# Performance work log

Measured on AMD Instinct MI355X. Metric: run time of the kernel, lower is better.

## Reference

```python
import jax, jax.numpy as jnp
import numpy as np

N = 100000   # nodes
R = 8        # relations
E = 150000   # edges per relation
D_IN = 128
D_OUT = 128
B = 2        # num_bases


def setup_inputs() -> dict:
    key = jax.random.key(0)
    ks = jax.random.split(key, 7)
    return {
        "x": jax.random.normal(ks[0], (N, D_IN), dtype=jnp.float32),
        "src": jax.random.randint(ks[1], (R, E), 0, N, dtype=jnp.int32),
        "dst": jax.random.randint(ks[2], (R, E), 0, N, dtype=jnp.int32),
        "basis_coeff": jax.random.normal(ks[3], (R, B), dtype=jnp.float32),
        "bases": jax.random.normal(ks[4], (B, D_IN, D_OUT), dtype=jnp.float32) * 0.05,
        "loop_weight": jax.random.normal(ks[5], (D_IN, D_OUT), dtype=jnp.float32) * 0.05,
        "h_bias": jax.random.normal(ks[6], (D_OUT,), dtype=jnp.float32) * 0.01,
    }


def reference(x, src, dst, basis_coeff, bases, loop_weight, h_bias):
    n = x.shape[0]
    # basis-decomposed per-relation weights: [R, D_IN, D_OUT]
    weight = jnp.einsum('rb,bio->rio', basis_coeff, bases)
    # gather src features per relation: [R, E, D_IN]
    msgs = x[src]
    # scatter-add onto dst nodes per relation (SpMM aggregate): [R, N, D_IN]
    agg = jax.vmap(lambda m, d: jax.ops.segment_sum(m, d, num_segments=n))(msgs, dst)
    # right normalization: divide by in-degree (clamped to 1), as in DGL GraphConv norm='right'
    ones = jnp.ones(src.shape[1], dtype=x.dtype)
    deg = jax.vmap(lambda d: jax.ops.segment_sum(ones, d, num_segments=n))(dst)
    agg = agg / jnp.clip(deg, 1.0)[..., None]
    # per-relation weight then sum across relations (HeteroGraphConv 'sum' agg)
    h = jnp.einsum('rni,rio->no', agg, weight)
    # self-loop + bias + activation (dropout = 0.0, eval)
    h = h + x @ loop_weight + h_bias
    return jax.nn.relu(h)
```

## Files before the change

### kernel.cpp

```cpp
#include <hip/hip_runtime.h>
#include <hip/hip_fp16.h>


#define DFEAT 128
#define NREL 8
#define ALDA 264
#define ECAP 512

typedef __attribute__((ext_vector_type(8))) short bf16x8;
typedef __attribute__((ext_vector_type(4))) float f32x4;
typedef __attribute__((ext_vector_type(2))) float f32x2;

__device__ __forceinline__ ushort f2bf(float f) {
    unsigned u = __float_as_uint(f);
    u += 0x7FFF + ((u >> 16) & 1);
    return (ushort)(u >> 16);
}
__device__ __forceinline__ float bflo(unsigned u) { return __uint_as_float(u << 16); }
__device__ __forceinline__ float bfhi(unsigned u) { return __uint_as_float(u & 0xFFFF0000u); }
__device__ __forceinline__ unsigned pack2bf(float lo, float hi) {
    return (unsigned)f2bf(lo) | ((unsigned)f2bf(hi) << 16);
}

__global__ void fused_pre(const int* __restrict__ dst, int* __restrict__ deg,
                          ushort* __restrict__ rank,
                          const float* __restrict__ x, ushort* __restrict__ xb,
                          const float* __restrict__ bases, const float* __restrict__ loopw,
                          ushort* __restrict__ w2T,
                          int RE, int E, int N, int n4) {
    const int stride = gridDim.x * blockDim.x;
    const int t0 = blockIdx.x * blockDim.x + threadIdx.x;
    for (int i = t0; i < RE; i += stride) {
        int r = i / E;
        int d = dst[i];
        rank[i] = (ushort)atomicAdd(&deg[r * N + d], 1);
    }
    for (int i = t0; i < n4; i += stride) {
        float4 v = ((const float4*)x)[i];
        ushort4 o;
        o.x = f2bf(v.x); o.y = f2bf(v.y); o.z = f2bf(v.z); o.w = f2bf(v.w);
        ((ushort4*)xb)[i] = o;
    }
    for (int i = t0; i < 128 * 384; i += stride) {
        int j = i / 384, k = i % 384;
        float v = (k < 256) ? bases[(k >> 7) * DFEAT * DFEAT + (k & 127) * DFEAT + j]
                            : loopw[(k - 256) * DFEAT + j];
        w2T[i] = f2bf(v);
    }
}

__global__ void scan_block_sums(const int* __restrict__ deg,
                                int* __restrict__ bsums, int N) {
    __shared__ int sdata[256];
    int b = blockIdx.x, t = threadIdx.x;
    int idx = b * 256 + t;
    int sum = 0;
    if (idx < N) {
        #pragma unroll
        for (int r = 0; r < NREL; ++r) sum += deg[r * N + idx];
    }
    sdata[t] = sum; __syncthreads();
    for (int s = 128; s > 0; s >>= 1) {
        if (t < s) sdata[t] += sdata[t + s];
        __syncthreads();
    }
    if (t == 0) bsums[b] = sdata[0];
}

__global__ void scan_write(const int* __restrict__ bsums,
                           const int* __restrict__ deg,
                           int* __restrict__ rowStart, unsigned* __restrict__ packed,
                           int N) {
    __shared__ int sdata[256];
    int b = blockIdx.x, t = threadIdx.x;

    int part = 0;
    for (int k = t; k < b; k += 256) part += bsums[k];
    sdata[t] = part; __syncthreads();
    for (int s = 128; s > 0; s >>= 1) {
        if (t < s) sdata[t] += sdata[t + s];
        __syncthreads();
    }
    const int boff = sdata[0];
    __syncthreads();

    int idx = b * 256 + t;
    int dvs[NREL];
    int c = 0;
    if (idx < N) {
        #pragma unroll
        for (int r = 0; r < NREL; ++r) { dvs[r] = deg[r * N + idx]; c += dvs[r]; }
    }
    sdata[t] = c; __syncthreads();
    for (int off = 1; off < 256; off <<= 1) {
        int x = 0;
        if (t >= off) x = sdata[t - off];
        __syncthreads();
        if (t >= off) sdata[t] += x;
        __syncthreads();
    }
    int excl = sdata[t] - c;
    if (idx < N) {
        int rs = boff + excl;
        rowStart[idx] = rs;
        int pre = 0;
        #pragma unroll
        for (int r = 0; r < NREL; ++r) {
            int dv = dvs[r];
            packed[r * N + idx] = ((unsigned)(rs + pre) << 11) | (unsigned)dv;
            pre += dv;
        }
    }
}

__global__ void fill_kernel(const int* __restrict__ src, const int* __restrict__ dst,
                            const ushort* __restrict__ rank,
                            const unsigned* __restrict__ packed,
                            unsigned* __restrict__ recs, int RE, int E, int N) {
    int idx = blockIdx.x * blockDim.x + threadIdx.x;
    if (idx >= RE) return;
    int r = idx / E;
    int d = dst[idx];
    unsigned p = packed[r * N + d];
    int pos = (int)(p >> 11) + (int)rank[idx];
    recs[pos] = (unsigned)src[idx] | ((unsigned)r << 17);
}

__global__ __launch_bounds__(256, 7) void gather_gemm(
    const unsigned* __restrict__ recs, const int* __restrict__ rowStart,
    const int* __restrict__ deg, const float* __restrict__ coeff,
    const ushort* __restrict__ xb,
    const ushort* __restrict__ w2T, const float* __restrict__ bias,
    float* __restrict__ out, int N, int RE) {
    __shared__ __align__(16) ushort agg[32 * ALDA];
    __shared__ __align__(16) unsigned recsL[ECAP];
    __shared__ float2 ccL[32 * NREL];
    __shared__ int rsl[33];
    const int tid = threadIdx.x;
    const int wave = tid >> 6, lane = tid & 63;
    const int row0 = blockIdx.x * 32;

    if (tid < 33) {
        int d = row0 + tid;
        rsl[tid] = (d < N) ? rowStart[d] : RE;
    }
    {
        int i = tid & 31, r = tid >> 5;
        int d = row0 + i;
        float2 cc = {0.f, 0.f};
        if (d < N) {
            int dv = deg[r * N + d];
            float inv = (dv > 0) ? 1.0f / (float)dv : 0.f;
            cc.x = coeff[2 * r] * inv;
            cc.y = coeff[2 * r + 1] * inv;
        }
        ccL[i * NREL + r] = cc;
    }
    __syncthreads();
    const int e0 = rsl[0];
    const int cntE = rsl[32] - e0;
    const bool fits = (cntE <= ECAP);
    {
        const int lim = fits ? cntE : 0;
        for (int k = tid; k < lim; k += 256)
            recsL[k] = recs[e0 + k];
    }
    __syncthreads();

    {
        const int qw = tid >> 4;
        const int h  = tid & 15;

        auto gatherNode = [&](int i, auto getRec) {
            const int s   = rsl[i] - e0;
            const int len = rsl[i + 1] - rsl[i];
            f32x2 A0 = {0.f,0.f}, A1 = {0.f,0.f}, A2 = {0.f,0.f}, A3 = {0.f,0.f};
            f32x2 B0 = {0.f,0.f}, B1 = {0.f,0.f}, B2 = {0.f,0.f}, B3 = {0.f,0.f};
            if (len > 0) {
                const int last = s + len - 1;
                for (int k = 0; k < len; k += 8) {
                    unsigned rc[8];
                    #pragma unroll
                    for (int j = 0; j < 8; ++j) {
                        int li = s + k + j;
                        rc[j] = getRec(li <= last ? li : last);
                    }
                    uint4 u[8];
                    #pragma unroll
                    for (int j = 0; j < 8; ++j)
                        u[j] = *(const uint4*)(xb + (size_t)(rc[j] & 0x1FFFFu) * DFEAT + h * 8);
                    #pragma unroll
                    for (int j = 0; j < 8; ++j) {
                        bool v = (k + j) < len;
                        float2 cf = ccL[i * NREL + (rc[j] >> 17)];
                        float c0 = v ? cf.x : 0.f;
                        float c1 = v ? cf.y : 0.f;
                        f32x2 cc0 = {c0, c0}, cc1 = {c1, c1};
                        uint4 uu = u[j];
                        f32x2 f01 = {bflo(uu.x), bfhi(uu.x)};
                        f32x2 f23 = {bflo(uu.y), bfhi(uu.y)};
                        f32x2 f45 = {bflo(uu.z), bfhi(uu.z)};
                        f32x2 f67 = {bflo(uu.w), bfhi(uu.w)};
                        A0 += cc0 * f01; A1 += cc0 * f23; A2 += cc0 * f45; A3 += cc0 * f67;
                        B0 += cc1 * f01; B1 += cc1 * f23; B2 += cc1 * f45; B3 += cc1 * f67;
                    }
                }
            }
            uint4 w0, w1;
            w0.x = pack2bf(A0.x, A0.y); w0.y = pack2bf(A1.x, A1.y);
            w0.z = pack2bf(A2.x, A2.y); w0.w = pack2bf(A3.x, A3.y);
            w1.x = pack2bf(B0.x, B0.y); w1.y = pack2bf(B1.x, B1.y);
            w1.z = pack2bf(B2.x, B2.y); w1.w = pack2bf(B3.x, B3.y);
            *(uint4*)(agg + i * ALDA + h * 8)       = w0;
            *(uint4*)(agg + i * ALDA + 128 + h * 8) = w1;
        };

        if (fits) {
            #pragma unroll
            for (int p = 0; p < 2; ++p)
                gatherNode(qw + p * 16, [&](int li) { return recsL[li]; });
        } else {
            #pragma unroll
            for (int p = 0; p < 2; ++p)
                gatherNode(qw + p * 16, [&](int li) { return recs[e0 + li]; });
        }
    }
    __syncthreads();

    const int quad = lane >> 4, l16 = lane & 15;
    int arow[2];
    #pragma unroll
    for (int m = 0; m < 2; ++m) {
        int r = row0 + m * 16 + l16;
        arow[m] = (r < N) ? r : 0;
    }

    f32x4 zero = {0.f, 0.f, 0.f, 0.f};
    f32x4 acc[2][2] = {{zero, zero}, {zero, zero}};

    #pragma unroll
    for (int kt = 0; kt < 3; ++kt) {
        bf16x8 bq[4][2];
        #pragma unroll
        for (int t = 0; t < 4; ++t)
            #pragma unroll
            for (int g = 0; g < 2; ++g)
                bq[t][g] = *(const bf16x8*)(w2T + (size_t)(wave * 32 + g * 16 + l16) * 384
                                            + kt * 128 + t * 32 + quad * 8);
        #pragma unroll
        for (int m = 0; m < 2; ++m) {
            #pragma unroll
            for (int t = 0; t < 4; ++t) {
                bf16x8 a;
                if (kt < 2)
                    a = *(const bf16x8*)(agg + (m * 16 + l16) * ALDA + kt * 128 + t * 32 + quad * 8);
                else
                    a = *(const bf16x8*)(xb + (size_t)arow[m] * DFEAT + t * 32 + quad * 8);
                acc[m][0] = __builtin_amdgcn_mfma_f32_16x16x32_bf16(a, bq[t][0], acc[m][0], 0, 0, 0);
                acc[m][1] = __builtin_amdgcn_mfma_f32_16x16x32_bf16(a, bq[t][1], acc[m][1], 0, 0, 0);
            }
        }
    }

    #pragma unroll
    for (int g = 0; g < 2; ++g) {
        int c = wave * 32 + g * 16 + l16;
        float bv = bias[c];
        #pragma unroll
        for (int m = 0; m < 2; ++m) {
            #pragma unroll
            for (int reg = 0; reg < 4; ++reg) {
                int grow = row0 + m * 16 + quad * 4 + reg;
                if (grow < N)
                    out[(size_t)grow * DFEAT + c] = fmaxf(acc[m][g][reg] + bv, 0.f);
            }
        }
    }
}

extern "C" void kernel_launch(void* const* d_in, const int* in_sizes, int n_in,
                              void* d_out, int out_size, void* d_ws, size_t ws_size,
                              hipStream_t stream) {
    const float* x     = (const float*)d_in[0];
    const int*   src   = (const int*)  d_in[1];
    const int*   dst   = (const int*)  d_in[2];
    const float* coeff = (const float*)d_in[3];
    const float* bases = (const float*)d_in[4];
    const float* loopw = (const float*)d_in[5];
    const float* bias  = (const float*)d_in[6];
    float* out = (float*)d_out;

    const int N  = in_sizes[0] / DFEAT;
    const int RE = in_sizes[1];
    const int B  = in_sizes[4] / (DFEAT * DFEAT);
    const int R  = in_sizes[3] / B;
    const int E  = RE / R;
    const int NB = (N + 255) / 256;
    const int n4 = N * 32;

    char* ws = (char*)d_ws;
    size_t off = 0;
    auto alloc = [&](size_t bytes) { void* p = ws + off; off = (off + bytes + 255) & ~(size_t)255; return p; };
    int*      deg      = (int*)     alloc((size_t)R * N * sizeof(int));
    ushort*   rank     = (ushort*)  alloc((size_t)RE * sizeof(ushort));
    unsigned* packed   = (unsigned*)alloc((size_t)R * N * sizeof(unsigned));
    int*      rowStart = (int*)     alloc((size_t)N * sizeof(int));
    int*      bsums    = (int*)     alloc((size_t)NB * sizeof(int));
    ushort*   w2T      = (ushort*)  alloc((size_t)128 * 384 * sizeof(ushort));
    ushort*   xb       = (ushort*)  alloc((size_t)N * DFEAT * sizeof(ushort));
    unsigned* recs     = (unsigned*)alloc((size_t)RE * sizeof(unsigned));

    hipMemsetAsync(deg, 0, (size_t)R * N * sizeof(int), stream);
    fused_pre<<<4096, 256, 0, stream>>>(dst, deg, rank, x, xb, bases, loopw, w2T,
                                        RE, E, N, n4);
    scan_block_sums<<<NB, 256, 0, stream>>>(deg, bsums, N);
    scan_write<<<NB, 256, 0, stream>>>(bsums, deg, rowStart, packed, N);
    fill_kernel<<<(RE + 255) / 256, 256, 0, stream>>>(src, dst, rank, packed,
                                                      recs, RE, E, N);
    gather_gemm<<<(N + 31) / 32, 256, 0, stream>>>(recs, rowStart, deg, coeff,
                                                   xb, w2T, bias, out, N, RE);
}
```

Before: 279.7 us.

## Replace atomic-degree CSR build with two-level bucketed radix sort of edges

Builds the destination-sorted edge list with a two-level counting sort instead of global atomics. Edges are first bucketed by the high bits of dst (512-node buckets) using per-block shared-memory histograms and a column scan, then each bucket is sorted locally in shared memory, which also computes degrees and row starts. This removes the full-size degree memset, the per-edge global atomics with rank storage, and the packed offset table. In exchange it adds an extra pass over the edge records and an intermediate buffer, and the order of edges within a row now depends on atomic ordering.

```diff
diff --git a/kernel.cpp b/kernel.cpp
--- a/kernel.cpp
+++ b/kernel.cpp
@@ -6,6 +6,8 @@
 #define NREL 8
 #define ALDA 264
 #define ECAP 512
+#define BSH 9
+#define EPB 1024
 
 typedef __attribute__((ext_vector_type(8))) short bf16x8;
 typedef __attribute__((ext_vector_type(4))) float f32x4;
@@ -22,26 +24,37 @@
     return (unsigned)f2bf(lo) | ((unsigned)f2bf(hi) << 16);
 }
 
-__global__ void fused_pre(const int* __restrict__ dst, int* __restrict__ deg,
-                          ushort* __restrict__ rank,
-                          const float* __restrict__ x, ushort* __restrict__ xb,
-                          const float* __restrict__ bases, const float* __restrict__ loopw,
-                          ushort* __restrict__ w2T,
-                          int RE, int E, int N, int n4) {
+__global__ void k1_hist_conv(const int* __restrict__ dst,
+                             const float* __restrict__ x, ushort* __restrict__ xb,
+                             const float* __restrict__ bases, const float* __restrict__ loopw,
+                             ushort* __restrict__ w2T,
+                             int* __restrict__ bh, int* __restrict__ tot,
+                             int RE, int N, int n4, int B1, int NBUCK) {
+    __shared__ int hist[256];
+    const int b = blockIdx.x, t = threadIdx.x;
+    hist[t] = 0;
+    __syncthreads();
+    const int e0 = b * EPB;
+    #pragma unroll
+    for (int j = 0; j < EPB / 256; ++j) {
+        int i = e0 + j * 256 + t;
+        if (i < RE) atomicAdd(&hist[dst[i] >> BSH], 1);
+    }
+    __syncthreads();
+    if (t < NBUCK) {
+        int h = hist[t];
+        bh[t * B1 + b] = h;
+        if (h) atomicAdd(&tot[t], h);
+    }
     const int stride = gridDim.x * blockDim.x;
-    const int t0 = blockIdx.x * blockDim.x + threadIdx.x;
-    for (int i = t0; i < RE; i += stride) {
-        int r = i / E;
-        int d = dst[i];
-        rank[i] = (ushort)atomicAdd(&deg[r * N + d], 1);
-    }
-    for (int i = t0; i < n4; i += stride) {
+    const int gt = b * 256 + t;
+    for (int i = gt; i < n4; i += stride) {
         float4 v = ((const float4*)x)[i];
         ushort4 o;
         o.x = f2bf(v.x); o.y = f2bf(v.y); o.z = f2bf(v.z); o.w = f2bf(v.w);
         ((ushort4*)xb)[i] = o;
     }
-    for (int i = t0; i < 128 * 384; i += stride) {
+    for (int i = gt; i < 128 * 384; i += stride) {
         int j = i / 384, k = i % 384;
         float v = (k < 256) ? bases[(k >> 7) * DFEAT * DFEAT + (k & 127) * DFEAT + j]
                             : loopw[(k - 256) * DFEAT + j];
@@ -49,81 +62,125 @@
     }
 }
 
-__global__ void scan_block_sums(const int* __restrict__ deg,
-                                int* __restrict__ bsums, int N) {
-    __shared__ int sdata[256];
-    int b = blockIdx.x, t = threadIdx.x;
-    int idx = b * 256 + t;
-    int sum = 0;
-    if (idx < N) {
-        #pragma unroll
-        for (int r = 0; r < NREL; ++r) sum += deg[r * N + idx];
-    }
-    sdata[t] = sum; __syncthreads();
-    for (int s = 128; s > 0; s >>= 1) {
-        if (t < s) sdata[t] += sdata[t + s];
-        __syncthreads();
-    }
-    if (t == 0) bsums[b] = sdata[0];
-}
-
-__global__ void scan_write(const int* __restrict__ bsums,
-                           const int* __restrict__ deg,
-                           int* __restrict__ rowStart, unsigned* __restrict__ packed,
-                           int N) {
-    __shared__ int sdata[256];
-    int b = blockIdx.x, t = threadIdx.x;
-
+__global__ void k2_scan(int* __restrict__ bh, const int* __restrict__ tot,
+                        int B1, int NBUCK) {
+    __shared__ int s[256];
+    __shared__ int carry;
+    const int bu = blockIdx.x, t = threadIdx.x;
     int part = 0;
-    for (int k = t; k < b; k += 256) part += bsums[k];
-    sdata[t] = part; __syncthreads();
-    for (int s = 128; s > 0; s >>= 1) {
-        if (t < s) sdata[t] += sdata[t + s];
-        __syncthreads();
-    }
-    const int boff = sdata[0];
-    __syncthreads();
-
-    int idx = b * 256 + t;
-    int dvs[NREL];
-    int c = 0;
-    if (idx < N) {
-        #pragma unroll
-        for (int r = 0; r < NREL; ++r) { dvs[r] = deg[r * N + idx]; c += dvs[r]; }
-    }
-    sdata[t] = c; __syncthreads();
+    for (int k = t; k < bu; k += 256) part += tot[k];
+    s[t] = part; __syncthreads();
+    for (int off = 128; off > 0; off >>= 1) {
+        if (t < off) s[t] += s[t + off];
+        __syncthreads();
+    }
+    if (t == 0) carry = s[0];
+    __syncthreads();
+    int* col = bh + (size_t)bu * B1;
+    for (int base = 0; base < B1; base += 256) {
+        int idx = base + t;
+        int v = (idx < B1) ? col[idx] : 0;
+        s[t] = v; __syncthreads();
+        for (int off = 1; off < 256; off <<= 1) {
+            int x = (t >= off) ? s[t - off] : 0;
+            __syncthreads();
+            s[t] += x;
+            __syncthreads();
+        }
+        if (idx < B1) col[idx] = carry + s[t] - v;
+        __syncthreads();
+        if (t == 0) carry += s[255];
+        __syncthreads();
+    }
+}
+
+__global__ void k3_scatter(const int* __restrict__ src, const int* __restrict__ dst,
+                           const int* __restrict__ bh, unsigned* __restrict__ recsC,
+                           int RE, int E, int B1, int NBUCK) {
+    __shared__ int cursor[256];
+    const int b = blockIdx.x, t = threadIdx.x;
+    if (t < NBUCK) cursor[t] = bh[t * B1 + b];
+    __syncthreads();
+    const int e0 = b * EPB;
+    #pragma unroll
+    for (int j = 0; j < EPB / 256; ++j) {
+        int i = e0 + j * 256 + t;
+        if (i < RE) {
+            int d = dst[i];
+            int r = i / E;
+            int slot = atomicAdd(&cursor[d >> BSH], 1);
+            recsC[slot] = (unsigned)src[i] | ((unsigned)r << 17)
+                        | ((unsigned)(d & 511) << 20);
+        }
+    }
+}
+
+__global__ void k4_bucket(const unsigned* __restrict__ recsC,
+                          const int* __restrict__ tot,
+                          int* __restrict__ rowStart, int* __restrict__ deg,
+                          unsigned* __restrict__ recs, int N, int NBUCK) {
+    __shared__ int cnt[512];
+    __shared__ int degL[512 * NREL];
+    __shared__ int scanS[256];
+    __shared__ int start[512];
+    const int bu = blockIdx.x, t = threadIdx.x;
+
+    int part = 0;
+    for (int k = t; k < bu; k += 256) part += tot[k];
+    scanS[t] = part; __syncthreads();
+    for (int off = 128; off > 0; off >>= 1) {
+        if (t < off) scanS[t] += scanS[t + off];
+        __syncthreads();
+    }
+    const int base = scanS[0];
+    __syncthreads();
+    const int end = base + tot[bu];
+
+    cnt[t] = 0; cnt[t + 256] = 0;
+    for (int k = t; k < 512 * NREL; k += 256) degL[k] = 0;
+    __syncthreads();
+
+    for (int e = base + t; e < end; e += 256) {
+        unsigned rc = recsC[e];
+        int dloc = rc >> 20;
+        int r = (rc >> 17) & 7;
+        atomicAdd(&cnt[dloc], 1);
+        atomicAdd(&degL[dloc * NREL + r], 1);
+    }
+    __syncthreads();
+
+    int c0 = cnt[2 * t], c1 = cnt[2 * t + 1];
+    int ps = c0 + c1;
+    scanS[t] = ps; __syncthreads();
     for (int off = 1; off < 256; off <<= 1) {
-        int x = 0;
-        if (t >= off) x = sdata[t - off];
-        __syncthreads();
-        if (t >= off) sdata[t] += x;
-        __syncthreads();
-    }
-    int excl = sdata[t] - c;
-    if (idx < N) {
-        int rs = boff + excl;
-        rowStart[idx] = rs;
-        int pre = 0;
-        #pragma unroll
-        for (int r = 0; r < NREL; ++r) {
-            int dv = dvs[r];
-            packed[r * N + idx] = ((unsigned)(rs + pre) << 11) | (unsigned)dv;
-            pre += dv;
-        }
-    }
-}
-
-__global__ void fill_kernel(const int* __restrict__ src, const int* __restrict__ dst,
-                            const ushort* __restrict__ rank,
-                            const unsigned* __restrict__ packed,
-                            unsigned* __restrict__ recs, int RE, int E, int N) {
-    int idx = blockIdx.x * blockDim.x + threadIdx.x;
-    if (idx >= RE) return;
-    int r = idx / E;
-    int d = dst[idx];
-    unsigned p = packed[r * N + d];
-    int pos = (int)(p >> 11) + (int)rank[idx];
-    recs[pos] = (unsigned)src[idx] | ((unsigned)r << 17);
+        int x = (t >= off) ? scanS[t - off] : 0;
+        __syncthreads();
+        scanS[t] += x;
+        __syncthreads();
+    }
+    int excl = scanS[t] - ps;
+    start[2 * t] = excl;
+    start[2 * t + 1] = excl + c0;
+    __syncthreads();
+
+    const int d0 = bu << BSH;
+    { int d = d0 + t;       if (d < N) rowStart[d] = base + start[t]; }
+    { int d = d0 + 256 + t; if (d < N) rowStart[d] = base + start[256 + t]; }
+    for (int k = t; k < 512 * NREL; k += 256) {
+        int d = d0 + (k >> 3);
+        int r = k & 7;
+        if (d < N) deg[r * N + d] = degL[k];
+    }
+    __syncthreads();
+    cnt[t] = start[t]; cnt[t + 256] = start[t + 256];
+    __syncthreads();
+
+    for (int e = base + t; e < end; e += 256) {
+        unsigned rc = recsC[e];
+        int dloc = rc >> 20;
+        int slot = base + atomicAdd(&cnt[dloc], 1);
+        recs[slot] = rc & 0xFFFFFu;
+    }
 }
 
 __global__ __launch_bounds__(256, 7) void gather_gemm(
@@ -295,28 +352,28 @@
     const int B  = in_sizes[4] / (DFEAT * DFEAT);
     const int R  = in_sizes[3] / B;
     const int E  = RE / R;
-    const int NB = (N + 255) / 256;
     const int n4 = N * 32;
+    const int NBUCK = (N + 511) >> BSH;
+    const int B1 = (RE + EPB - 1) / EPB;
 
     char* ws = (char*)d_ws;
     size_t off = 0;
     auto alloc = [&](size_t bytes) { void* p = ws + off; off = (off + bytes + 255) & ~(size_t)255; return p; };
     int*      deg      = (int*)     alloc((size_t)R * N * sizeof(int));
-    ushort*   rank     = (ushort*)  alloc((size_t)RE * sizeof(ushort));
-    unsigned* packed   = (unsigned*)alloc((size_t)R * N * sizeof(unsigned));
     int*      rowStart = (int*)     alloc((size_t)N * sizeof(int));
-    int*      bsums    = (int*)     alloc((size_t)NB * sizeof(int));
+    int*      tot      = (int*)     alloc((size_t)NBUCK * sizeof(int));
+    int*      bh       = (int*)     alloc((size_t)NBUCK * B1 * sizeof(int));
     ushort*   w2T      = (ushort*)  alloc((size_t)128 * 384 * sizeof(ushort));
     ushort*   xb       = (ushort*)  alloc((size_t)N * DFEAT * sizeof(ushort));
+    unsigned* recsC    = (unsigned*)alloc((size_t)RE * sizeof(unsigned));
     unsigned* recs     = (unsigned*)alloc((size_t)RE * sizeof(unsigned));
 
-    hipMemsetAsync(deg, 0, (size_t)R * N * sizeof(int), stream);
-    fused_pre<<<4096, 256, 0, stream>>>(dst, deg, rank, x, xb, bases, loopw, w2T,
-                                        RE, E, N, n4);
-    scan_block_sums<<<NB, 256, 0, stream>>>(deg, bsums, N);
-    scan_write<<<NB, 256, 0, stream>>>(bsums, deg, rowStart, packed, N);
-    fill_kernel<<<(RE + 255) / 256, 256, 0, stream>>>(src, dst, rank, packed,
-                                                      recs, RE, E, N);
+    hipMemsetAsync(tot, 0, (size_t)NBUCK * sizeof(int), stream);
+    k1_hist_conv<<<B1, 256, 0, stream>>>(dst, x, xb, bases, loopw, w2T,
+                                         bh, tot, RE, N, n4, B1, NBUCK);
+    k2_scan<<<NBUCK, 256, 0, stream>>>(bh, tot, B1, NBUCK);
+    k3_scatter<<<B1, 256, 0, stream>>>(src, dst, bh, recsC, RE, E, B1, NBUCK);
+    k4_bucket<<<NBUCK, 256, 0, stream>>>(recsC, tot, rowStart, deg, recs, N, NBUCK);
     gather_gemm<<<(N + 31) / 32, 256, 0, stream>>>(recs, rowStart, deg, coeff,
                                                    xb, w2T, bias, out, N, RE);
 }
```

New measurement: 273.2 us. 1.02x faster.
